# Optimization experiments

Measured on AMD Instinct MI355X. Metric: run time of the kernel, lower is better.

Reference implementation:

```python
import math
import jax, jax.numpy as jnp
import numpy as np

D_K = 64  # matches init d_k, used for the 1/sqrt(d_k) scale


def setup_inputs() -> dict:
    key = jax.random.key(0)
    k1, k2, k3, k4 = jax.random.split(key, 4)
    B, H, S, D = 4, 8, 4096, 64
    Q = jax.random.normal(k1, (B, H, S, D), dtype=jnp.float32)
    K = jax.random.normal(k2, (B, H, S, D), dtype=jnp.float32)
    V = jax.random.normal(k3, (B, H, S, D), dtype=jnp.float32)
    attn_mask = jax.random.randint(k4, (B, H, S, S), 0, 2).astype(jnp.bool_)
    return {"Q": Q, "K": K, "V": V, "attn_mask": attn_mask}


def _log_inds(l_k: int) -> np.ndarray:
    log_l_k = int(math.log2(l_k))
    return np.array([l_k - 2 ** (log_l_k - i) for i in range(log_l_k)], dtype=np.int32)


def reference(Q, K, V, attn_mask):
    l_k = K.shape[2]
    inds = jnp.asarray(_log_inds(l_k))  # static, shape [log2(l_k)]
    K_g = K[:, :, inds, :]               # [b,h,log_l_k,d]
    V_g = V[:, :, inds, :]               # [b,h,log_l_k,d]
    scores = jnp.einsum('bhqd,bhkd->bhqk', Q, K_g) / jnp.sqrt(jnp.float32(D_K))
    if attn_mask is not None:
        mask_g = attn_mask[:, :, :, inds]
        scores = jnp.where(mask_g, jnp.float32(-1e9), scores)
    attn = jax.nn.softmax(scores, axis=-1)  # [b,h,q,log_l_k]
    context = jnp.einsum('bhqk,bhkd->bhqd', attn, V_g)
    return (context, attn)
```

## Files before the change

### kernel.cpp

```cpp
#include <hip/hip_runtime.h>

constexpr int S   = 4096;
constexpr int D   = 64;
constexpr int NK  = 12;
constexpr int TPB = 256;
constexpr int BH  = 32;
constexpr long long CTX_ELEMS = (long long)BH * S * D;

__device__ __forceinline__ int log_ind(int k) { return S - (S >> k); }

__global__ __launch_bounds__(TPB, 2)
void logtrans_kernel(const float* __restrict__ Qg,
                     const float* __restrict__ Kg,
                     const float* __restrict__ Vg,
                     const int*   __restrict__ maskg,
                     float*       __restrict__ out_ctx,
                     float*       __restrict__ out_attn)
{
    __shared__ float kls[NK * D];
    __shared__ float vls[NK * D];

    const int t    = threadIdx.x;
    const int row0 = blockIdx.x * TPB;
    const int bh   = row0 >> 12;
    const long long kvbase = (long long)bh * (S * D);

    for (int e = t; e < NK * D; e += TPB) {
        const int k = e >> 6;
        const int d = e & 63;
        const long long off = kvbase + (long long)log_ind(k) * D + d;
        kls[e] = Kg[off];
        vls[e] = Vg[off];
    }
    __syncthreads();

    const int r = row0 + t;

    float q[D];
    const float4* q16 = (const float4*)(Qg + (long long)r * D);
    #pragma unroll
    for (int i = 0; i < D / 4; ++i) {
        float4 u = q16[i];
        q[4*i+0] = u.x; q[4*i+1] = u.y; q[4*i+2] = u.z; q[4*i+3] = u.w;
    }

    float sc[NK];
    #pragma unroll
    for (int k = 0; k < NK; ++k) {
        const float4* kp = (const float4*)(kls + k * D);
        float dot = 0.f;
        #pragma unroll
        for (int i = 0; i < D / 4; ++i) {
            float4 kv = kp[i];
            dot += q[4*i+0] * kv.x;
            dot += q[4*i+1] * kv.y;
            dot += q[4*i+2] * kv.z;
            dot += q[4*i+3] * kv.w;
        }
        sc[k] = dot * 0.125f;
    }

    const long long mbase = (long long)r * S;
    #pragma unroll
    for (int k = 0; k < NK; ++k) {
        if (maskg[mbase + log_ind(k)] != 0) sc[k] = -1.0e9f;
    }

    float m = sc[0];
    #pragma unroll
    for (int k = 1; k < NK; ++k) m = fmaxf(m, sc[k]);
    float a[NK];
    float sum = 0.f;
    #pragma unroll
    for (int k = 0; k < NK; ++k) { a[k] = __expf(sc[k] - m); sum += a[k]; }
    const float inv = 1.0f / sum;
    #pragma unroll
    for (int k = 0; k < NK; ++k) a[k] *= inv;

    float4* oa = (float4*)(out_attn + (long long)r * NK);
    #pragma unroll
    for (int k = 0; k < 3; ++k) {
        float4 p;
        p.x = a[4*k+0]; p.y = a[4*k+1]; p.z = a[4*k+2]; p.w = a[4*k+3];
        oa[k] = p;
    }

    float4* oc = (float4*)(out_ctx + (long long)r * D);
    #pragma unroll
    for (int i = 0; i < D / 4; ++i) {
        float ax = 0.f, ay = 0.f, az = 0.f, aw = 0.f;
        #pragma unroll
        for (int k = 0; k < NK; ++k) {
            float4 vv = ((const float4*)(vls + k * D))[i];
            ax += a[k] * vv.x;
            ay += a[k] * vv.y;
            az += a[k] * vv.z;
            aw += a[k] * vv.w;
        }
        float4 p; p.x = ax; p.y = ay; p.z = az; p.w = aw;
        oc[i] = p;
    }
}

extern "C" void kernel_launch(void* const* d_in, const int* in_sizes, int n_in,
                              void* d_out, int out_size, void* d_ws, size_t ws_size,
                              hipStream_t stream) {
    const float* Q    = (const float*)d_in[0];
    const float* K    = (const float*)d_in[1];
    const float* V    = (const float*)d_in[2];
    const int*   mask = (const int*)d_in[3];
    float* out_ctx  = (float*)d_out;
    float* out_attn = out_ctx + CTX_ELEMS;

    const int total_rows = BH * S;
    logtrans_kernel<<<dim3(total_rows / TPB), dim3(TPB), 0, stream>>>(
        Q, K, V, mask, out_ctx, out_attn);
}
```

Before: 2.451 ms.

## Stage Q and context through padded LDS for coalesced loads and stores

Q rows are loaded cooperatively into padded shared memory with coalesced float4 reads, then each thread reads its own row from LDS. Context outputs are written back through the same LDS buffer so global stores are coalesced. Mask loads are issued before the barrier, with the last two indices fetched in one int4. The aim is to avoid strided per-thread 256-byte row accesses, at the cost of about 66KB of LDS per block, which reduces occupancy, plus extra barriers.

```diff
diff --git a/kernel.cpp b/kernel.cpp
--- a/kernel.cpp
+++ b/kernel.cpp
@@ -5,6 +5,7 @@
 constexpr int NK  = 12;
 constexpr int TPB = 256;
 constexpr int BH  = 32;
+constexpr int QSTRIDE = D + 1;
 constexpr long long CTX_ELEMS = (long long)BH * S * D;
 
 __device__ __forceinline__ int log_ind(int k) { return S - (S >> k); }
@@ -19,30 +20,48 @@
 {
     __shared__ float kls[NK * D];
     __shared__ float vls[NK * D];
+    __shared__ float qs[TPB * QSTRIDE];
 
     const int t    = threadIdx.x;
     const int row0 = blockIdx.x * TPB;
     const int bh   = row0 >> 12;
     const long long kvbase = (long long)bh * (S * D);
 
-    for (int e = t; e < NK * D; e += TPB) {
-        const int k = e >> 6;
-        const int d = e & 63;
-        const long long off = kvbase + (long long)log_ind(k) * D + d;
-        kls[e] = Kg[off];
-        vls[e] = Vg[off];
+    for (int e = t; e < 2 * NK * (D / 4); e += TPB) {
+        const int m  = e >= NK * (D / 4);
+        const int i  = m ? e - NK * (D / 4) : e;
+        const int k  = i >> 4;
+        const int d4 = (i & 15) * 4;
+        const float* src = (m ? Vg : Kg) + kvbase + (long long)log_ind(k) * D + d4;
+        float4 v = *(const float4*)src;
+        float* dst = (m ? vls : kls) + k * D + d4;
+        dst[0] = v.x; dst[1] = v.y; dst[2] = v.z; dst[3] = v.w;
     }
+
+    const float4* qsrc = (const float4*)(Qg + (long long)row0 * D);
+    #pragma unroll
+    for (int j = 0; j < 16; ++j) {
+        const int e  = j * TPB + t;
+        float4 v = qsrc[e];
+        float* dst = qs + (e >> 4) * QSTRIDE + (e & 15) * 4;
+        dst[0] = v.x; dst[1] = v.y; dst[2] = v.z; dst[3] = v.w;
+    }
+
+    const long long mbase = (long long)(row0 + t) * S;
+    int mk[NK];
+    #pragma unroll
+    for (int k = 0; k < 10; ++k) mk[k] = maskg[mbase + log_ind(k)];
+    {
+        int4 tail = *(const int4*)(maskg + mbase + 4092);
+        mk[10] = tail.x;
+        mk[11] = tail.z;
+    }
+
     __syncthreads();
 
-    const int r = row0 + t;
-
     float q[D];
-    const float4* q16 = (const float4*)(Qg + (long long)r * D);
     #pragma unroll
-    for (int i = 0; i < D / 4; ++i) {
-        float4 u = q16[i];
-        q[4*i+0] = u.x; q[4*i+1] = u.y; q[4*i+2] = u.z; q[4*i+3] = u.w;
-    }
+    for (int d = 0; d < D; ++d) q[d] = qs[t * QSTRIDE + d];
 
     float sc[NK];
     #pragma unroll
@@ -52,18 +71,10 @@
         #pragma unroll
         for (int i = 0; i < D / 4; ++i) {
             float4 kv = kp[i];
-            dot += q[4*i+0] * kv.x;
-            dot += q[4*i+1] * kv.y;
-            dot += q[4*i+2] * kv.z;
-            dot += q[4*i+3] * kv.w;
+            dot += q[4*i+0] * kv.x + q[4*i+1] * kv.y
+                 + q[4*i+2] * kv.z + q[4*i+3] * kv.w;
         }
-        sc[k] = dot * 0.125f;
-    }
-
-    const long long mbase = (long long)r * S;
-    #pragma unroll
-    for (int k = 0; k < NK; ++k) {
-        if (maskg[mbase + log_ind(k)] != 0) sc[k] = -1.0e9f;
+        sc[k] = mk[k] ? -1.0e9f : dot * 0.125f;
     }
 
     float m = sc[0];
@@ -77,7 +88,7 @@
     #pragma unroll
     for (int k = 0; k < NK; ++k) a[k] *= inv;
 
-    float4* oa = (float4*)(out_attn + (long long)r * NK);
+    float4* oa = (float4*)(out_attn + (long long)(row0 + t) * NK);
     #pragma unroll
     for (int k = 0; k < 3; ++k) {
         float4 p;
@@ -85,20 +96,32 @@
         oa[k] = p;
     }
 
-    float4* oc = (float4*)(out_ctx + (long long)r * D);
+    float c[D];
     #pragma unroll
     for (int i = 0; i < D / 4; ++i) {
         float ax = 0.f, ay = 0.f, az = 0.f, aw = 0.f;
         #pragma unroll
         for (int k = 0; k < NK; ++k) {
             float4 vv = ((const float4*)(vls + k * D))[i];
-            ax += a[k] * vv.x;
-            ay += a[k] * vv.y;
-            az += a[k] * vv.z;
-            aw += a[k] * vv.w;
+            ax += a[k] * vv.x; ay += a[k] * vv.y;
+            az += a[k] * vv.z; aw += a[k] * vv.w;
         }
-        float4 p; p.x = ax; p.y = ay; p.z = az; p.w = aw;
-        oc[i] = p;
+        c[4*i+0] = ax; c[4*i+1] = ay; c[4*i+2] = az; c[4*i+3] = aw;
+    }
+
+    __syncthreads();
+    #pragma unroll
+    for (int d = 0; d < D; ++d) qs[t * QSTRIDE + d] = c[d];
+    __syncthreads();
+
+    float4* cdst = (float4*)(out_ctx + (long long)row0 * D);
+    #pragma unroll
+    for (int j = 0; j < 16; ++j) {
+        const int e = j * TPB + t;
+        const float* sp = qs + (e >> 4) * QSTRIDE + (e & 15) * 4;
+        float4 v;
+        v.x = sp[0]; v.y = sp[1]; v.z = sp[2]; v.w = sp[3];
+        cdst[e] = v;
     }
 }
 
```

After: 2.338 ms. 4.6% less time.

## Split each query row across four lanes with shuffle-reduced dot products

Applied to the files above, without the earlier changes.

Each row is now handled by four threads. Each thread loads a strided quarter of Q as float4, computes partial dot products, and reduces them with xor shuffles. Mask lookups are spread across the lanes and merged into a bitmask, and the K/V shared loads use float4 and are issued before the barrier to overlap with the Q and mask fetches. This lowers per-thread register use so more blocks can be resident (launch bounds raised to 6) and makes the Q and context accesses coalesced, at the cost of extra shuffles and four times as many blocks each reloading K/V.

```diff
diff --git a/kernel.cpp b/kernel.cpp
--- a/kernel.cpp
+++ b/kernel.cpp
@@ -4,12 +4,13 @@
 constexpr int D   = 64;
 constexpr int NK  = 12;
 constexpr int TPB = 256;
+constexpr int RPB = TPB / 4;
 constexpr int BH  = 32;
 constexpr long long CTX_ELEMS = (long long)BH * S * D;
 
 __device__ __forceinline__ int log_ind(int k) { return S - (S >> k); }
 
-__global__ __launch_bounds__(TPB, 2)
+__global__ __launch_bounds__(TPB, 6)
 void logtrans_kernel(const float* __restrict__ Qg,
                      const float* __restrict__ Kg,
                      const float* __restrict__ Vg,
@@ -17,88 +18,86 @@
                      float*       __restrict__ out_ctx,
                      float*       __restrict__ out_attn)
 {
-    __shared__ float kls[NK * D];
-    __shared__ float vls[NK * D];
+    __shared__ float4 kls[NK * 16];
+    __shared__ float4 vls[NK * 16];
 
     const int t    = threadIdx.x;
-    const int row0 = blockIdx.x * TPB;
-    const int bh   = row0 >> 12;
+    const int l    = t & 3;
+    const int rq   = t >> 2;
+    const int row0 = blockIdx.x * RPB;
+    const int r    = row0 + rq;
+    const int bh   = r >> 12;
     const long long kvbase = (long long)bh * (S * D);
 
-    for (int e = t; e < NK * D; e += TPB) {
-        const int k = e >> 6;
-        const int d = e & 63;
-        const long long off = kvbase + (long long)log_ind(k) * D + d;
-        kls[e] = Kg[off];
-        vls[e] = Vg[off];
+    for (int e = t; e < 2 * NK * 16; e += TPB) {
+        const int mKV = e >= NK * 16;
+        const int i   = mKV ? e - NK * 16 : e;
+        const int k   = i >> 4;
+        const int d4  = i & 15;
+        const float4 v = *(const float4*)((mKV ? Vg : Kg) + kvbase
+                                          + (long long)log_ind(k) * D + d4 * 4);
+        (mKV ? vls : kls)[i] = v;
     }
+
+    float4 q4[4];
+    const float4* qrow = (const float4*)(Qg + (long long)r * D);
+    #pragma unroll
+    for (int j = 0; j < 4; ++j) q4[j] = qrow[l + 4 * j];
+
+    unsigned mb = 0;
+    const long long mbase = (long long)r * S;
+    #pragma unroll
+    for (int m = 0; m < 3; ++m) {
+        const int k = l + 4 * m;
+        if (maskg[mbase + log_ind(k)] != 0) mb |= (1u << k);
+    }
+    mb |= __shfl_xor(mb, 1);
+    mb |= __shfl_xor(mb, 2);
+
     __syncthreads();
-
-    const int r = row0 + t;
-
-    float q[D];
-    const float4* q16 = (const float4*)(Qg + (long long)r * D);
-    #pragma unroll
-    for (int i = 0; i < D / 4; ++i) {
-        float4 u = q16[i];
-        q[4*i+0] = u.x; q[4*i+1] = u.y; q[4*i+2] = u.z; q[4*i+3] = u.w;
-    }
 
     float sc[NK];
     #pragma unroll
     for (int k = 0; k < NK; ++k) {
-        const float4* kp = (const float4*)(kls + k * D);
-        float dot = 0.f;
+        const float4* kp = kls + k * 16;
+        float p = 0.f;
         #pragma unroll
-        for (int i = 0; i < D / 4; ++i) {
-            float4 kv = kp[i];
-            dot += q[4*i+0] * kv.x;
-            dot += q[4*i+1] * kv.y;
-            dot += q[4*i+2] * kv.z;
-            dot += q[4*i+3] * kv.w;
+        for (int j = 0; j < 4; ++j) {
+            float4 kv = kp[l + 4 * j];
+            p += q4[j].x * kv.x + q4[j].y * kv.y + q4[j].z * kv.z + q4[j].w * kv.w;
         }
-        sc[k] = dot * 0.125f;
-    }
-
-    const long long mbase = (long long)r * S;
-    #pragma unroll
-    for (int k = 0; k < NK; ++k) {
-        if (maskg[mbase + log_ind(k)] != 0) sc[k] = -1.0e9f;
+        p += __shfl_xor(p, 1);
+        p += __shfl_xor(p, 2);
+        sc[k] = ((mb >> k) & 1u) ? -1.0e9f : p * 0.125f;
     }
 
     float m = sc[0];
     #pragma unroll
     for (int k = 1; k < NK; ++k) m = fmaxf(m, sc[k]);
-    float a[NK];
     float sum = 0.f;
     #pragma unroll
-    for (int k = 0; k < NK; ++k) { a[k] = __expf(sc[k] - m); sum += a[k]; }
+    for (int k = 0; k < NK; ++k) { sc[k] = __expf(sc[k] - m); sum += sc[k]; }
     const float inv = 1.0f / sum;
     #pragma unroll
-    for (int k = 0; k < NK; ++k) a[k] *= inv;
+    for (int k = 0; k < NK; ++k) sc[k] *= inv;
 
-    float4* oa = (float4*)(out_attn + (long long)r * NK);
-    #pragma unroll
-    for (int k = 0; k < 3; ++k) {
-        float4 p;
-        p.x = a[4*k+0]; p.y = a[4*k+1]; p.z = a[4*k+2]; p.w = a[4*k+3];
-        oa[k] = p;
+    if (l < 3) {
+        float4 av;
+        av.x = sc[4*l+0]; av.y = sc[4*l+1]; av.z = sc[4*l+2]; av.w = sc[4*l+3];
+        ((float4*)(out_attn + (long long)r * NK))[l] = av;
     }
 
-    float4* oc = (float4*)(out_ctx + (long long)r * D);
+    float4* crow = (float4*)(out_ctx + (long long)r * D);
     #pragma unroll
-    for (int i = 0; i < D / 4; ++i) {
-        float ax = 0.f, ay = 0.f, az = 0.f, aw = 0.f;
+    for (int j = 0; j < 4; ++j) {
+        float4 acc; acc.x = acc.y = acc.z = acc.w = 0.f;
         #pragma unroll
         for (int k = 0; k < NK; ++k) {
-            float4 vv = ((const float4*)(vls + k * D))[i];
-            ax += a[k] * vv.x;
-            ay += a[k] * vv.y;
-            az += a[k] * vv.z;
-            aw += a[k] * vv.w;
+            float4 vv = vls[k * 16 + l + 4 * j];
+            acc.x += sc[k] * vv.x; acc.y += sc[k] * vv.y;
+            acc.z += sc[k] * vv.z; acc.w += sc[k] * vv.w;
         }
-        float4 p; p.x = ax; p.y = ay; p.z = az; p.w = aw;
-        oc[i] = p;
+        crow[l + 4 * j] = acc;
     }
 }
 
@@ -113,6 +112,6 @@
     float* out_attn = out_ctx + CTX_ELEMS;
 
     const int total_rows = BH * S;
-    logtrans_kernel<<<dim3(total_rows / TPB), dim3(TPB), 0, stream>>>(
+    logtrans_kernel<<<dim3(total_rows / RPB), dim3(TPB), 0, stream>>>(
         Q, K, V, mask, out_ctx, out_attn);
 }
```

Result: no change. 2.424 ms (-1.1%).
